# Kernel optimization log

Measured on AMD Instinct MI355X. Metric: run time of the kernel, lower is better.

Reference implementation:

```python
import jax, jax.numpy as jnp
import numpy as np

N = 50000   # nodes
E = 800000  # edges (avg degree 16)
H = 256     # hidden_dim
OUT = 256   # out_dim


def _leaky(x, slope=0.01):
    return jnp.where(x >= 0, x, slope * x)


def _mlp3(x, W1, b1, W2, b2, W3, b3):
    # MLP(hidden, hidden/2, hidden/2, hidden) with LeakyReLU(0.01) between layers
    x = _leaky(x @ W1 + b1)
    x = _leaky(x @ W2 + b2)
    return x @ W3 + b3


def setup_inputs() -> dict:
    key = jax.random.key(0)
    ks = jax.random.split(key, 16)
    Hh = H // 2

    def w(k, i, o):
        return (jax.random.normal(k, (i, o), jnp.float32) / np.float32(np.sqrt(i)))

    return {
        'h': jax.random.normal(ks[0], (N, H), jnp.float32),
        'src': jax.random.randint(ks[1], (E,), 0, N, dtype=jnp.int32),
        'dst': jax.random.randint(ks[2], (E,), 0, N, dtype=jnp.int32),
        'r': jax.random.randint(ks[3], (E,), 0, 2, dtype=jnp.int32),
        'inv': jax.random.randint(ks[4], (N,), 0, 2, dtype=jnp.int32),
        'inv_W1': w(ks[5], H, Hh), 'inv_b1': jnp.zeros((Hh,), jnp.float32),
        'inv_W2': w(ks[6], Hh, Hh), 'inv_b2': jnp.zeros((Hh,), jnp.float32),
        'inv_W3': w(ks[7], Hh, H), 'inv_b3': jnp.zeros((H,), jnp.float32),
        'and_W1': w(ks[8], H, Hh), 'and_b1': jnp.zeros((Hh,), jnp.float32),
        'and_W2': w(ks[9], Hh, Hh), 'and_b2': jnp.zeros((Hh,), jnp.float32),
        'and_W3': w(ks[10], Hh, H), 'and_b3': jnp.zeros((H,), jnp.float32),
        'proj_W1': w(ks[11], H, H), 'proj_b1': jnp.zeros((H,), jnp.float32),
        'proj_W2': w(ks[12], H, OUT), 'proj_b2': jnp.zeros((OUT,), jnp.float32),
    }


def reference(h, src, dst, r, inv,
              inv_W1, inv_b1, inv_W2, inv_b2, inv_W3, inv_b3,
              and_W1, and_b1, and_W2, and_b2, and_W3, and_b3,
              proj_W1, proj_b1, proj_W2, proj_b2):
    # edge_msg: gather src features, apply func_inv on edges with r == 1
    msg = h[src]  # [E, H]
    msg = jnp.where((r == 1)[:, None],
                    _mlp3(msg, inv_W1, inv_b1, inv_W2, inv_b2, inv_W3, inv_b3),
                    msg)
    # fn.mean('m', 'neigh'): mean over incoming edges per destination node
    sums = jax.ops.segment_sum(msg, dst, num_segments=N)          # [N, H]
    cnt = jax.ops.segment_sum(jnp.ones((E,), msg.dtype), dst, num_segments=N)
    neigh = sums / jnp.maximum(cnt, 1.0)[:, None]
    # apply_nodes_func: func_and, then func_inv where inv flag set
    res = _mlp3(neigh, and_W1, and_b1, and_W2, and_b2, and_W3, and_b3)
    res = jnp.where((inv == 1)[:, None],
                    _mlp3(res, inv_W1, inv_b1, inv_W2, inv_b2, inv_W3, inv_b3),
                    res)
    # proj_head: MLP(H, H, OUT) with negative_slope=0 (i.e. ReLU)
    out = jax.nn.relu(res @ proj_W1 + proj_b1) @ proj_W2 + proj_b2
    return out
```

## Files before the change

### kernel.cpp

```cpp
#include <hip/hip_runtime.h>

typedef _Float16 f16_t;
typedef f16_t f16x2 __attribute__((ext_vector_type(2)));
typedef f16_t f16x4 __attribute__((ext_vector_type(4)));
typedef f16_t f16x8 __attribute__((ext_vector_type(8)));
typedef float f32x4 __attribute__((ext_vector_type(4)));
typedef float f32x16 __attribute__((ext_vector_type(16)));

#define MFMA16H(a, b, c) __builtin_amdgcn_mfma_f32_16x16x32_f16(a, b, c, 0, 0, 0)
#define MFMA32H(a, b, c) __builtin_amdgcn_mfma_f32_32x32x16_f16(a, b, c, 0, 0, 0)

__device__ __forceinline__ float leaky01(float v) { return v >= 0.f ? v : 0.01f * v; }

__device__ __forceinline__ void acc_f16x4(float& s0, float& s1, float& s2, float& s3,
                                          f16x4 v)
{
#if __has_builtin(__builtin_amdgcn_fdot2)
    const f16x2 K10 = (f16x2){(f16_t)1.0f, (f16_t)0.0f};
    const f16x2 K01 = (f16x2){(f16_t)0.0f, (f16_t)1.0f};
    f16x2 lo = (f16x2){v.x, v.y};
    f16x2 hi = (f16x2){v.z, v.w};
    s0 = __builtin_amdgcn_fdot2(lo, K10, s0, false);
    s1 = __builtin_amdgcn_fdot2(lo, K01, s1, false);
    s2 = __builtin_amdgcn_fdot2(hi, K10, s2, false);
    s3 = __builtin_amdgcn_fdot2(hi, K01, s3, false);
#else
    s0 += (float)v.x; s1 += (float)v.y; s2 += (float)v.z; s3 += (float)v.w;
#endif
}

#define OFF_IW1 0
#define OFF_IW2 32768
#define OFF_IW3 49152
#define OFF_AW1 81920
#define OFF_AW2 114688
#define OFF_AW3 131072
#define OFF_PW1 163840
#define OFF_PW2 229376
#define OFF_M3  294912
#define WP_TOTAL 311296

template<int KD, int NC>
__device__ __forceinline__ void gemm16(
    const f16_t* __restrict__ a, int sa, const f16_t* __restrict__ B,
    int cb, int qd, int ln, f32x4 (&acc)[2])
{
    acc[0] = (f32x4){0.f, 0.f, 0.f, 0.f};
    acc[1] = acc[0];
#pragma unroll
    for (int k0 = 0; k0 < KD; k0 += 32) {
        int ka = k0 + qd * 8;
        f16x8 b = *(const f16x8*)(B + ((size_t)((k0 >> 5) * 4 + qd) * NC + cb + ln) * 8);
        f16x8 a0 = *(const f16x8*)&a[ln * sa + ka];
        f16x8 a1 = *(const f16x8*)&a[(16 + ln) * sa + ka];
        acc[0] = MFMA16H(a0, b, acc[0]);
        acc[1] = MFMA16H(a1, b, acc[1]);
    }
}

template<int KD, int NC>
__device__ __forceinline__ void gemm32(
    const f16_t* __restrict__ a, int sa, const f16_t* __restrict__ B,
    int cb, int l31, int kh, f32x16 &o)
{
    f32x16 c;
#pragma unroll
    for (int i = 0; i < 16; ++i) c[i] = 0.f;
    const int ar = l31 * sa + kh * 8;
    const int bcol = cb + l31;
#pragma unroll
    for (int kc = 0; kc < KD; kc += 32) {
        f16x8 b0 = *(const f16x8*)(B + ((size_t)((kc >> 3) + kh) * NC + bcol) * 8);
        f16x8 b1 = *(const f16x8*)(B + ((size_t)((kc >> 3) + 2 + kh) * NC + bcol) * 8);
        f16x8 a0 = *(const f16x8*)&a[ar + kc];
        f16x8 a1 = *(const f16x8*)&a[ar + kc + 16];
        c = MFMA32H(a0, b0, c);
        c = MFMA32H(a1, b1, c);
    }
    o = c;
}

template<int ACT>
__device__ __forceinline__ void epi16(
    f32x4 (&acc)[2], const float* __restrict__ bias,
    int cb, int qd, int ln, f16_t* d, int stride)
{
    int col = cb + ln;
    float bb = bias[col];
#pragma unroll
    for (int rt = 0; rt < 2; ++rt)
#pragma unroll
        for (int r = 0; r < 4; ++r) {
            float v = acc[rt][r] + bb;
            if (ACT == 1) v = leaky01(v);
            else if (ACT == 2) v = fmaxf(v, 0.f);
            d[(rt * 16 + qd * 4 + r) * stride + col] = (f16_t)v;
        }
}

template<int ACT>
__device__ __forceinline__ void epi32(
    const f32x16 &a0, const float* __restrict__ bias,
    int cb, int l31, int kh, f16_t* d, int stride)
{
    int col = cb + l31;
    float bb = bias[col];
#pragma unroll
    for (int r = 0; r < 16; ++r) {
        float v = a0[r] + bb;
        if (ACT == 1) v = leaky01(v);
        else if (ACT == 2) v = fmaxf(v, 0.f);
        int row = (r & 3) + 8 * (r >> 2) + 4 * kh;
        d[row * stride + col] = (f16_t)v;
    }
}

__global__ __launch_bounds__(512) void prep_kernel(
    const float* s0, const float* s1, const float* s2, const float* s3,
    const float* s4, const float* s5, const float* s6, const float* s7,
    const float* __restrict__ ib3, f16_t* dst, float* __restrict__ c3f,
    const int* __restrict__ dstE, int* __restrict__ cnt, int E)
{
    const int tid = threadIdx.x;
    const int bid = blockIdx.x;

    if (bid < 1024) {
        const float* srcs[8] = {s0, s1, s2, s3, s4, s5, s6, s7};
        const int lgN[8] = {7, 7, 8, 7, 7, 8, 8, 8};
        const int sz[8]  = {32768, 16384, 32768, 32768, 16384, 32768, 65536, 65536};
        const int off[8] = {OFF_IW1, OFF_IW2, OFF_IW3, OFF_AW1, OFF_AW2, OFF_AW3,
                            OFF_PW1, OFF_PW2};
        int m = bid >> 7;
        int idx = (bid & 127) * 512 + tid;
        if (idx >= sz[m]) return;
        int lg = lgN[m];
        int Nc = 1 << lg;
        int k = idx >> lg;
        int n = idx & (Nc - 1);
        int p = ((k >> 3) * Nc + n) * 8 + (k & 7);
        dst[off[m] + p] = (f16_t)srcs[m][idx];
    } else if (bid < 1056) {
        int idx = (bid - 1024) * 512 + tid;
        int k = idx >> 7, j = idx & 127;
        float s = 0.f;
        for (int t = 0; t < 256; ++t) s += s2[k * 256 + t] * s3[t * 128 + j];
        int p = ((k >> 3) * 128 + j) * 8 + (k & 7);
        dst[OFF_M3 + p] = (f16_t)s;
    } else if (bid == 1056) {
        int j = tid;
        if (j < 128) {
            float s = 0.f;
            for (int t = 0; t < 256; ++t) s += ib3[t] * s3[t * 128 + j];
            c3f[j] = s;
        }
    } else {
        int e = (bid - 1057) * 512 + tid;
        if (e < E) atomicAdd(&cnt[dstE[e]], 1);
    }
}

__global__ void scan1(const int* __restrict__ cnt, int* __restrict__ offs,
                      int* __restrict__ bsum, int Nn)
{
    __shared__ int s[256];
    int tid = threadIdx.x;
    int g = blockIdx.x * 256 + tid;
    int v = (g < Nn) ? cnt[g] : 0;
    s[tid] = v;
    __syncthreads();
    for (int off = 1; off < 256; off <<= 1) {
        int u = (tid >= off) ? s[tid - off] : 0;
        __syncthreads();
        s[tid] += u;
        __syncthreads();
    }
    if (g < Nn) offs[g] = s[tid] - v;
    if (tid == 255) bsum[blockIdx.x] = s[255];
}

__global__ void scan3b(int* __restrict__ offs, const int* __restrict__ bsum,
                       int* __restrict__ cursor, int Nn, int NB)
{
    __shared__ int s[256];
    int tid = threadIdx.x;
    int bid = blockIdx.x;
    int v = (tid < NB) ? bsum[tid] : 0;
    s[tid] = v;
    __syncthreads();
    for (int off = 1; off < 256; off <<= 1) {
        int u = (tid >= off) ? s[tid - off] : 0;
        __syncthreads();
        s[tid] += u;
        __syncthreads();
    }
    int base = (bid > 0) ? s[bid - 1] : 0;
    int g = bid * 256 + tid;
    if (g < Nn) {
        int o = offs[g] + base;
        offs[g] = o;
        cursor[g] = o;
    }
}

__global__ void scan2(int* __restrict__ bsum, int NB)
{
    if (threadIdx.x == 0) {
        int run = 0;
        for (int i = 0; i < NB; ++i) { int v = bsum[i]; bsum[i] = run; run += v; }
    }
}

__global__ void scan3(int* __restrict__ offs, const int* __restrict__ bsum,
                      int* __restrict__ cursor, int Nn)
{
    int g = blockIdx.x * 256 + threadIdx.x;
    if (g < Nn) {
        int o = offs[g] + bsum[blockIdx.x];
        offs[g] = o;
        cursor[g] = o;
    }
}

__global__ __launch_bounds__(512, 8) void fillA(
    const float* __restrict__ h, f16_t* __restrict__ zbuf,
    const f16_t* __restrict__ wp, const float* __restrict__ ib1,
    const float* __restrict__ ib2, const float* __restrict__ c3f, int M,
    int tiles, const int* __restrict__ dstE, const int* __restrict__ srcE,
    const int* __restrict__ rE, int* __restrict__ cursor,
    int* __restrict__ ridx, int E)
{
    __shared__ f16_t X[32][264];
    __shared__ f16_t Y[32][136];

    const int tid = threadIdx.x;

    if ((int)blockIdx.x >= tiles) {
        int e = (blockIdx.x - tiles) * 512 + tid;
        if (e < E) {
            int p = atomicAdd(&cursor[dstE[e]], 1);
            ridx[p] = srcE[e] * 2 + rE[e];
        }
        return;
    }

    const int row0 = blockIdx.x * 32;
    const int lane = tid & 63;
    const int wv = tid >> 6;
    const int qd = lane >> 4;
    const int ln = lane & 15;
    const int cb = wv * 16;
    const int l31 = lane & 31;
    const int kh = lane >> 5;

    {
        const float4* src4 = (const float4*)(h + (size_t)row0 * 256);
#pragma unroll
        for (int i = 0; i < 4; ++i) {
            int q = i * 512 + tid;
            int row = q >> 6;
            int kc = (q & 63) * 4;
            float4 v = make_float4(0.f, 0.f, 0.f, 0.f);
            if (row0 + row < M) v = src4[q];
            *(f16x4*)&X[row][kc] = (f16x4){(f16_t)v.x, (f16_t)v.y, (f16_t)v.z, (f16_t)v.w};
        }
    }
    __syncthreads();

    {
        const bool isz = wv < 4;
        const int cb32 = (wv & 3) * 32;
        const f16_t* Bw = wp + (isz ? OFF_AW1 : OFF_IW1);
        f32x16 z;
        gemm32<256, 128>(&X[0][0], 264, Bw, cb32, l31, kh, z);
        __syncthreads();
        int col = cb32 + l31;
        if (isz) {
#pragma unroll
            for (int r = 0; r < 16; ++r) {
                int lrow = (r & 3) + 8 * (r >> 2) + 4 * kh;
                X[lrow][128 + col] = (f16_t)z[r];
            }
        } else {
            float bb = ib1[col];
#pragma unroll
            for (int r = 0; r < 16; ++r) {
                int lrow = (r & 3) + 8 * (r >> 2) + 4 * kh;
                Y[lrow][col] = (f16_t)leaky01(z[r] + bb);
            }
        }
    }
    __syncthreads();

    f32x4 a4[2];

    gemm16<128, 128>(&Y[0][0], 136, wp + OFF_IW2, cb, qd, ln, a4);
    epi16<1>(a4, ib2, cb, qd, ln, &X[0][0], 264);
    __syncthreads();

    gemm16<128, 128>(&X[0][0], 264, wp + OFF_M3, cb, qd, ln, a4);
    {
        int col = cb + ln;
        float bb = c3f[col];
#pragma unroll
        for (int rt = 0; rt < 2; ++rt)
#pragma unroll
            for (int r = 0; r < 4; ++r)
                Y[rt * 16 + qd * 4 + r][col] = (f16_t)(a4[rt][r] + bb);
    }
    __syncthreads();

#pragma unroll
    for (int i = 0; i < 2; ++i) {
        int q = i * 512 + tid;
        int node = q >> 5;
        int seg = q & 31;
        int row = row0 + node;
        if (row < M) {
            f16x8 v = (seg < 16) ? *(const f16x8*)&X[node][128 + seg * 8]
                                 : *(const f16x8*)&Y[node][(seg - 16) * 8];
            *(f16x8*)&zbuf[(size_t)row * 256 + seg * 8] = v;
        }
    }
}

__global__ __launch_bounds__(512, 8) void kernelB(
    const f16_t* __restrict__ zbuf, const int* __restrict__ ridx,
    const int* __restrict__ offs, const int* __restrict__ cnt,
    const float* __restrict__ ab1, const int* __restrict__ invf,
    float* __restrict__ out, const f16_t* __restrict__ wp,
    const float* __restrict__ ab2, const float* __restrict__ ab3,
    const float* __restrict__ ib1, const float* __restrict__ ib2,
    const float* __restrict__ ib3, const float* __restrict__ pb1,
    const float* __restrict__ pb2, int M)
{
    __shared__ f16_t C[32][264];
    __shared__ f16_t A[32][136];
    __shared__ f16_t B2[32][136];
    __shared__ int sflag[32];

    const int tid = threadIdx.x;
    const int row0 = blockIdx.x * 32;
    const int lane = tid & 63;
    const int wv = tid >> 6;
    const int qd = lane >> 4;
    const int ln = lane & 15;
    const int cb2 = wv * 16;
    const int l31 = lane & 31;
    const int kh = lane >> 5;
    const int cb32 = wv * 32;

    const int hw = tid >> 5;
    const int hl = tid & 31;
    const int hbase = lane & 32;
    const f16x4* zp4 = (const f16x4*)zbuf;

#pragma unroll
    for (int pass = 0; pass < 2; ++pass) {
        int nl = pass * 16 + hw;
        int row = row0 + nl;
        float s0 = 0.f, s1 = 0.f, s2 = 0.f, s3 = 0.f;
        int c = 0;
        if (row < M) {
            int beg = offs[row];
            c = cnt[row];
            for (int base = 0; base < c; base += 32) {
                int rem = c - base; if (rem > 32) rem = 32;
                int myr = (hl < rem) ? ridx[beg + base + hl] : 0;
                int j = 0;
                for (; j + 16 <= rem; j += 16) {
                    f16x4 v[16];
#pragma unroll
                    for (int i = 0; i < 16; ++i) {
                        int rr = __shfl(myr, hbase + j + i);
                        v[i] = zp4[(size_t)rr * 32 + hl];
                    }
#pragma unroll
                    for (int i = 0; i < 16; ++i)
                        acc_f16x4(s0, s1, s2, s3, v[i]);
                }
                for (; j + 8 <= rem; j += 8) {
                    f16x4 v[8];
#pragma unroll
                    for (int i = 0; i < 8; ++i) {
                        int rr = __shfl(myr, hbase + j + i);
                        v[i] = zp4[(size_t)rr * 32 + hl];
                    }
#pragma unroll
                    for (int i = 0; i < 8; ++i)
                        acc_f16x4(s0, s1, s2, s3, v[i]);
                }
                for (; j < rem; ++j) {
                    int rr = __shfl(myr, hbase + j);
                    f16x4 vv = zp4[(size_t)rr * 32 + hl];
                    acc_f16x4(s0, s1, s2, s3, vv);
                }
            }
        }
        float invc = 1.0f / fmaxf((float)c, 1.0f);
        float4 bv = *(const float4*)&ab1[hl * 4];
        float m0 = leaky01(s0 * invc + bv.x);
        float m1 = leaky01(s1 * invc + bv.y);
        float m2 = leaky01(s2 * invc + bv.z);
        float m3 = leaky01(s3 * invc + bv.w);
        *(f16x4*)&A[nl][hl * 4] = (f16x4){(f16_t)m0, (f16_t)m1, (f16_t)m2, (f16_t)m3};
    }
    if (tid < 32) {
        int rr = row0 + tid;
        sflag[tid] = (rr < M) ? invf[rr] : 0;
    }
    __syncthreads();

    f32x4 a4[2];
    f32x16 c32;

    gemm16<128, 128>(&A[0][0], 136, wp + OFF_AW2, cb2, qd, ln, a4);
    epi16<1>(a4, ab2, cb2, qd, ln, &B2[0][0], 136);
    __syncthreads();

    gemm32<128, 256>(&B2[0][0], 136, wp + OFF_AW3, cb32, l31, kh, c32);
    epi32<0>(c32, ab3, cb32, l31, kh, &C[0][0], 264);
    __syncthreads();

    gemm16<256, 128>(&C[0][0], 264, wp + OFF_IW1, cb2, qd, ln, a4);
    epi16<1>(a4, ib1, cb2, qd, ln, &A[0][0], 136);
    __syncthreads();

    gemm16<128, 128>(&A[0][0], 136, wp + OFF_IW2, cb2, qd, ln, a4);
    epi16<1>(a4, ib2, cb2, qd, ln, &B2[0][0], 136);
    __syncthreads();

    gemm32<128, 256>(&B2[0][0], 136, wp + OFF_IW3, cb32, l31, kh, c32);
    {
        int col = cb32 + l31;
        float bb = ib3[col];
#pragma unroll
        for (int r = 0; r < 16; ++r) {
            int lrow = (r & 3) + 8 * (r >> 2) + 4 * kh;
            if (sflag[lrow] == 1) C[lrow][col] = (f16_t)(c32[r] + bb);
        }
    }
    __syncthreads();

    gemm32<256, 256>(&C[0][0], 264, wp + OFF_PW1, cb32, l31, kh, c32);
    __syncthreads();
    epi32<2>(c32, pb1, cb32, l31, kh, &C[0][0], 264);
    __syncthreads();

    gemm32<256, 256>(&C[0][0], 264, wp + OFF_PW2, cb32, l31, kh, c32);
    {
        int col = cb32 + l31;
        float bb = pb2[col];
#pragma unroll
        for (int r = 0; r < 16; ++r) {
            int lrow = (r & 3) + 8 * (r >> 2) + 4 * kh;
            int row = row0 + lrow;
            if (row < M) out[(size_t)row * 256 + col] = c32[r] + bb;
        }
    }
}

extern "C" void kernel_launch(void* const* d_in, const int* in_sizes, int n_in,
                              void* d_out, int out_size, void* d_ws, size_t ws_size,
                              hipStream_t stream)
{
    const float* h   = (const float*)d_in[0];
    const int* src   = (const int*)d_in[1];
    const int* dst   = (const int*)d_in[2];
    const int* r     = (const int*)d_in[3];
    const int* inv   = (const int*)d_in[4];
    const float* iW1 = (const float*)d_in[5];
    const float* ib1 = (const float*)d_in[6];
    const float* iW2 = (const float*)d_in[7];
    const float* ib2 = (const float*)d_in[8];
    const float* iW3 = (const float*)d_in[9];
    const float* ib3 = (const float*)d_in[10];
    const float* aW1 = (const float*)d_in[11];
    const float* ab1 = (const float*)d_in[12];
    const float* aW2 = (const float*)d_in[13];
    const float* ab2 = (const float*)d_in[14];
    const float* aW3 = (const float*)d_in[15];
    const float* ab3 = (const float*)d_in[16];
    const float* pW1 = (const float*)d_in[17];
    const float* pb1 = (const float*)d_in[18];
    const float* pW2 = (const float*)d_in[19];
    const float* pb2 = (const float*)d_in[20];

    const int N = in_sizes[0] / 256;
    const int E = in_sizes[1];
    float* out = (float*)d_out;

    f16_t* zbuf = (f16_t*)d_ws;
    int* cnt    = (int*)(zbuf + (size_t)2 * N * 128);
    int* offs   = cnt + N;
    int* cursor = offs + N;
    int* bsum   = cursor + N;
    int* ridx   = bsum + 256;
    f16_t* wp   = (f16_t*)(ridx + E);
    float* c3f  = (float*)(wp + WP_TOTAL);

    (void)hipMemsetAsync(cnt, 0, (size_t)N * sizeof(int), stream);

    const int tiles = (N + 31) / 32;
    const int EB = (E + 511) / 512;
    const int NB = (N + 255) / 256;

    prep_kernel<<<1057 + EB, 512, 0, stream>>>(iW1, iW2, iW3, aW1, aW2, aW3,
                                               pW1, pW2, ib3, wp, c3f,
                                               dst, cnt, E);

    scan1<<<NB, 256, 0, stream>>>(cnt, offs, bsum, N);
    if (NB <= 256) {
        scan3b<<<NB, 256, 0, stream>>>(offs, bsum, cursor, N, NB);
    } else {
        scan2<<<1, 1, 0, stream>>>(bsum, NB);
        scan3<<<NB, 256, 0, stream>>>(offs, bsum, cursor, N);
    }

    fillA<<<tiles + EB, 512, 0, stream>>>(h, zbuf, wp, ib1, ib2, c3f, N,
                                          tiles, dst, src, r, cursor, ridx, E);

    kernelB<<<tiles, 512, 0, stream>>>(zbuf, ridx, offs, cnt, ab1, inv, out, wp,
                                       ab2, ab3, ib1, ib2, ib3, pb1, pb2, N);
}
```

Baseline: 323.0 us.

## Fuse all stages into one persistent cooperative kernel with grid syncs

Replaces the memset, prep, scan and two compute kernel launches with a single cooperative persistent kernel. Stages are separated by grid-wide syncs, and work units are distributed with grid-stride loops. The scan now uses 512-thread blocks. The intent is to remove per-launch overhead and inter-kernel gaps. In exchange, occupancy is capped at resident blocks, grid.sync costs are added, and the shared-memory union may limit occupancy. The old multi-kernel path is kept as a fallback.

```diff
diff --git a/kernel.cpp b/kernel.cpp
--- a/kernel.cpp
+++ b/kernel.cpp
@@ -1,4 +1,5 @@
 #include <hip/hip_runtime.h>
+#include <hip/hip_cooperative_groups.h>
 
 typedef _Float16 f16_t;
 typedef f16_t f16x2 __attribute__((ext_vector_type(2)));
@@ -115,15 +116,229 @@
     }
 }
 
-__global__ __launch_bounds__(512) void prep_kernel(
+__device__ __forceinline__ void kernelA_tile(
+    int tile, const float* __restrict__ h, f16_t* __restrict__ zbuf,
+    const f16_t* __restrict__ wp, const float* __restrict__ ib1,
+    const float* __restrict__ ib2, const float* __restrict__ c3f, int M,
+    f16_t (*X)[264], f16_t (*Y)[136], int tid)
+{
+    const int row0 = tile * 32;
+    const int lane = tid & 63;
+    const int wv = tid >> 6;
+    const int qd = lane >> 4;
+    const int ln = lane & 15;
+    const int cb = wv * 16;
+    const int l31 = lane & 31;
+    const int kh = lane >> 5;
+
+    {
+        const float4* src4 = (const float4*)(h + (size_t)row0 * 256);
+#pragma unroll
+        for (int i = 0; i < 4; ++i) {
+            int q = i * 512 + tid;
+            int row = q >> 6;
+            int kc = (q & 63) * 4;
+            float4 v = make_float4(0.f, 0.f, 0.f, 0.f);
+            if (row0 + row < M) v = src4[q];
+            *(f16x4*)&X[row][kc] = (f16x4){(f16_t)v.x, (f16_t)v.y, (f16_t)v.z, (f16_t)v.w};
+        }
+    }
+    __syncthreads();
+
+    {
+        const bool isz = wv < 4;
+        const int cb32 = (wv & 3) * 32;
+        const f16_t* Bw = wp + (isz ? OFF_AW1 : OFF_IW1);
+        f32x16 z;
+        gemm32<256, 128>(&X[0][0], 264, Bw, cb32, l31, kh, z);
+        __syncthreads();
+        int col = cb32 + l31;
+        if (isz) {
+#pragma unroll
+            for (int r = 0; r < 16; ++r) {
+                int lrow = (r & 3) + 8 * (r >> 2) + 4 * kh;
+                X[lrow][128 + col] = (f16_t)z[r];
+            }
+        } else {
+            float bb = ib1[col];
+#pragma unroll
+            for (int r = 0; r < 16; ++r) {
+                int lrow = (r & 3) + 8 * (r >> 2) + 4 * kh;
+                Y[lrow][col] = (f16_t)leaky01(z[r] + bb);
+            }
+        }
+    }
+    __syncthreads();
+
+    f32x4 a4[2];
+
+    gemm16<128, 128>(&Y[0][0], 136, wp + OFF_IW2, cb, qd, ln, a4);
+    epi16<1>(a4, ib2, cb, qd, ln, &X[0][0], 264);
+    __syncthreads();
+
+    gemm16<128, 128>(&X[0][0], 264, wp + OFF_M3, cb, qd, ln, a4);
+    {
+        int col = cb + ln;
+        float bb = c3f[col];
+#pragma unroll
+        for (int rt = 0; rt < 2; ++rt)
+#pragma unroll
+            for (int r = 0; r < 4; ++r)
+                Y[rt * 16 + qd * 4 + r][col] = (f16_t)(a4[rt][r] + bb);
+    }
+    __syncthreads();
+
+#pragma unroll
+    for (int i = 0; i < 2; ++i) {
+        int q = i * 512 + tid;
+        int node = q >> 5;
+        int seg = q & 31;
+        int row = row0 + node;
+        if (row < M) {
+            f16x8 v = (seg < 16) ? *(const f16x8*)&X[node][128 + seg * 8]
+                                 : *(const f16x8*)&Y[node][(seg - 16) * 8];
+            *(f16x8*)&zbuf[(size_t)row * 256 + seg * 8] = v;
+        }
+    }
+}
+
+__device__ __forceinline__ void kernelB_tile(
+    int tile, const f16_t* __restrict__ zbuf, const int* __restrict__ ridx,
+    const int* __restrict__ offs, const int* __restrict__ cnt,
+    const float* __restrict__ ab1, const int* __restrict__ invf,
+    float* __restrict__ out, const f16_t* __restrict__ wp,
+    const float* __restrict__ ab2, const float* __restrict__ ab3,
+    const float* __restrict__ ib1, const float* __restrict__ ib2,
+    const float* __restrict__ ib3, const float* __restrict__ pb1,
+    const float* __restrict__ pb2, int M,
+    f16_t (*C)[264], f16_t (*A)[136], f16_t (*B2)[136], int* sflag, int tid)
+{
+    const int row0 = tile * 32;
+    const int lane = tid & 63;
+    const int wv = tid >> 6;
+    const int qd = lane >> 4;
+    const int ln = lane & 15;
+    const int cb2 = wv * 16;
+    const int l31 = lane & 31;
+    const int kh = lane >> 5;
+    const int cb32 = wv * 32;
+
+    const int hw = tid >> 5;
+    const int hl = tid & 31;
+    const int hbase = lane & 32;
+    const f16x4* zp4 = (const f16x4*)zbuf;
+
+#pragma unroll
+    for (int pass = 0; pass < 2; ++pass) {
+        int nl = pass * 16 + hw;
+        int row = row0 + nl;
+        float s0 = 0.f, s1 = 0.f, s2 = 0.f, s3 = 0.f;
+        int c = 0;
+        if (row < M) {
+            int beg = offs[row];
+            c = cnt[row];
+            for (int base = 0; base < c; base += 32) {
+                int rem = c - base; if (rem > 32) rem = 32;
+                int myr = (hl < rem) ? ridx[beg + base + hl] : 0;
+                int j = 0;
+                for (; j + 16 <= rem; j += 16) {
+                    f16x4 v[16];
+#pragma unroll
+                    for (int i = 0; i < 16; ++i) {
+                        int rr = __shfl(myr, hbase + j + i);
+                        v[i] = zp4[(size_t)rr * 32 + hl];
+                    }
+#pragma unroll
+                    for (int i = 0; i < 16; ++i)
+                        acc_f16x4(s0, s1, s2, s3, v[i]);
+                }
+                for (; j + 8 <= rem; j += 8) {
+                    f16x4 v[8];
+#pragma unroll
+                    for (int i = 0; i < 8; ++i) {
+                        int rr = __shfl(myr, hbase + j + i);
+                        v[i] = zp4[(size_t)rr * 32 + hl];
+                    }
+#pragma unroll
+                    for (int i = 0; i < 8; ++i)
+                        acc_f16x4(s0, s1, s2, s3, v[i]);
+                }
+                for (; j < rem; ++j) {
+                    int rr = __shfl(myr, hbase + j);
+                    f16x4 vv = zp4[(size_t)rr * 32 + hl];
+                    acc_f16x4(s0, s1, s2, s3, vv);
+                }
+            }
+        }
+        float invc = 1.0f / fmaxf((float)c, 1.0f);
+        float4 bv = *(const float4*)&ab1[hl * 4];
+        float m0 = leaky01(s0 * invc + bv.x);
+        float m1 = leaky01(s1 * invc + bv.y);
+        float m2 = leaky01(s2 * invc + bv.z);
+        float m3 = leaky01(s3 * invc + bv.w);
+        *(f16x4*)&A[nl][hl * 4] = (f16x4){(f16_t)m0, (f16_t)m1, (f16_t)m2, (f16_t)m3};
+    }
+    if (tid < 32) {
+        int rr = row0 + tid;
+        sflag[tid] = (rr < M) ? invf[rr] : 0;
+    }
+    __syncthreads();
+
+    f32x4 a4[2];
+    f32x16 c32;
+
+    gemm16<128, 128>(&A[0][0], 136, wp + OFF_AW2, cb2, qd, ln, a4);
+    epi16<1>(a4, ab2, cb2, qd, ln, &B2[0][0], 136);
+    __syncthreads();
+
+    gemm32<128, 256>(&B2[0][0], 136, wp + OFF_AW3, cb32, l31, kh, c32);
+    epi32<0>(c32, ab3, cb32, l31, kh, &C[0][0], 264);
+    __syncthreads();
+
+    gemm16<256, 128>(&C[0][0], 264, wp + OFF_IW1, cb2, qd, ln, a4);
+    epi16<1>(a4, ib1, cb2, qd, ln, &A[0][0], 136);
+    __syncthreads();
+
+    gemm16<128, 128>(&A[0][0], 136, wp + OFF_IW2, cb2, qd, ln, a4);
+    epi16<1>(a4, ib2, cb2, qd, ln, &B2[0][0], 136);
+    __syncthreads();
+
+    gemm32<128, 256>(&B2[0][0], 136, wp + OFF_IW3, cb32, l31, kh, c32);
+    {
+        int col = cb32 + l31;
+        float bb = ib3[col];
+#pragma unroll
+        for (int r = 0; r < 16; ++r) {
+            int lrow = (r & 3) + 8 * (r >> 2) + 4 * kh;
+            if (sflag[lrow] == 1) C[lrow][col] = (f16_t)(c32[r] + bb);
+        }
+    }
+    __syncthreads();
+
+    gemm32<256, 256>(&C[0][0], 264, wp + OFF_PW1, cb32, l31, kh, c32);
+    __syncthreads();
+    epi32<2>(c32, pb1, cb32, l31, kh, &C[0][0], 264);
+    __syncthreads();
+
+    gemm32<256, 256>(&C[0][0], 264, wp + OFF_PW2, cb32, l31, kh, c32);
+    {
+        int col = cb32 + l31;
+        float bb = pb2[col];
+#pragma unroll
+        for (int r = 0; r < 16; ++r) {
+            int lrow = (r & 3) + 8 * (r >> 2) + 4 * kh;
+            int row = row0 + lrow;
+            if (row < M) out[(size_t)row * 256 + col] = c32[r] + bb;
+        }
+    }
+}
+
+__device__ __forceinline__ void prep_unit(
+    int bid, int tid,
     const float* s0, const float* s1, const float* s2, const float* s3,
     const float* s4, const float* s5, const float* s6, const float* s7,
-    const float* __restrict__ ib3, f16_t* dst, float* __restrict__ c3f,
-    const int* __restrict__ dstE, int* __restrict__ cnt, int E)
-{
-    const int tid = threadIdx.x;
-    const int bid = blockIdx.x;
-
+    const float* __restrict__ ib3, f16_t* dst, float* __restrict__ c3f)
+{
     if (bid < 1024) {
         const float* srcs[8] = {s0, s1, s2, s3, s4, s5, s6, s7};
         const int lgN[8] = {7, 7, 8, 7, 7, 8, 8, 8};
@@ -153,6 +368,131 @@
             for (int t = 0; t < 256; ++t) s += ib3[t] * s3[t * 128 + j];
             c3f[j] = s;
         }
+    }
+}
+
+struct MegaArgs {
+    const float *h;
+    const float *iW1, *ib1, *iW2, *ib2, *iW3, *ib3;
+    const float *aW1, *ab1, *aW2, *ab2, *aW3, *ab3;
+    const float *pW1, *pb1, *pW2, *pb2;
+    const int *src, *dst, *r, *invf;
+    f16_t *zbuf;
+    f16_t *wp;
+    float *c3f;
+    float *out;
+    int *cnt, *offs, *cursor, *bsum, *ridx;
+    int N, E, tiles, EB, NBc;
+};
+
+__global__ __launch_bounds__(512, 8) void mega(MegaArgs a)
+{
+    namespace cg = cooperative_groups;
+    cg::grid_group grid = cg::this_grid();
+    __shared__ union {
+        struct { f16_t X[32][264]; f16_t Y[32][136]; } pa;
+        struct { f16_t C[32][264]; f16_t A[32][136]; f16_t B2[32][136]; int sflag[32]; } pb;
+        int s[512];
+    } sh;
+    const int tid = threadIdx.x;
+    const int nb = gridDim.x;
+
+    for (int i = blockIdx.x * 512 + tid; i < a.N; i += nb * 512) a.cnt[i] = 0;
+    __threadfence();
+    grid.sync();
+
+    {
+        const int T1 = 1057 + a.EB;
+        for (int u = blockIdx.x; u < T1; u += nb) {
+            if (u < 1057) {
+                prep_unit(u, tid, a.iW1, a.iW2, a.iW3, a.aW1, a.aW2, a.aW3,
+                          a.pW1, a.pW2, a.ib3, a.wp, a.c3f);
+            } else {
+                int e = (u - 1057) * 512 + tid;
+                if (e < a.E) atomicAdd(&a.cnt[a.dst[e]], 1);
+            }
+        }
+    }
+    __threadfence();
+    grid.sync();
+
+    for (int u = blockIdx.x; u < a.NBc; u += nb) {
+        __syncthreads();
+        int g = u * 512 + tid;
+        int v = (g < a.N) ? a.cnt[g] : 0;
+        sh.s[tid] = v;
+        __syncthreads();
+        for (int off = 1; off < 512; off <<= 1) {
+            int t = (tid >= off) ? sh.s[tid - off] : 0;
+            __syncthreads();
+            sh.s[tid] += t;
+            __syncthreads();
+        }
+        if (g < a.N) a.offs[g] = sh.s[tid] - v;
+        if (tid == 511) a.bsum[u] = sh.s[511];
+    }
+    __threadfence();
+    grid.sync();
+
+    for (int u = blockIdx.x; u < a.NBc; u += nb) {
+        __syncthreads();
+        int v = (tid < a.NBc) ? a.bsum[tid] : 0;
+        sh.s[tid] = v;
+        __syncthreads();
+        for (int off = 1; off < 512; off <<= 1) {
+            int t = (tid >= off) ? sh.s[tid - off] : 0;
+            __syncthreads();
+            sh.s[tid] += t;
+            __syncthreads();
+        }
+        int base = (u > 0) ? sh.s[u - 1] : 0;
+        int g = u * 512 + tid;
+        if (g < a.N) {
+            int o = a.offs[g] + base;
+            a.offs[g] = o;
+            a.cursor[g] = o;
+        }
+    }
+    __threadfence();
+    grid.sync();
+
+    {
+        const int T4 = a.EB + a.tiles;
+        for (int u = blockIdx.x; u < T4; u += nb) {
+            if (u < a.EB) {
+                int e = u * 512 + tid;
+                if (e < a.E) {
+                    int p = atomicAdd(&a.cursor[a.dst[e]], 1);
+                    a.ridx[p] = a.src[e] * 2 + a.r[e];
+                }
+            } else {
+                __syncthreads();
+                kernelA_tile(u - a.EB, a.h, a.zbuf, a.wp, a.ib1, a.ib2, a.c3f,
+                             a.N, sh.pa.X, sh.pa.Y, tid);
+            }
+        }
+    }
+    __threadfence();
+    grid.sync();
+
+    for (int u = blockIdx.x; u < a.tiles; u += nb) {
+        __syncthreads();
+        kernelB_tile(u, a.zbuf, a.ridx, a.offs, a.cnt, a.ab1, a.invf, a.out,
+                     a.wp, a.ab2, a.ab3, a.ib1, a.ib2, a.ib3, a.pb1, a.pb2,
+                     a.N, sh.pb.C, sh.pb.A, sh.pb.B2, sh.pb.sflag, tid);
+    }
+}
+
+__global__ __launch_bounds__(512) void prep_kernel(
+    const float* s0, const float* s1, const float* s2, const float* s3,
+    const float* s4, const float* s5, const float* s6, const float* s7,
+    const float* __restrict__ ib3, f16_t* dst, float* __restrict__ c3f,
+    const int* __restrict__ dstE, int* __restrict__ cnt, int E)
+{
+    const int tid = threadIdx.x;
+    const int bid = blockIdx.x;
+    if (bid < 1057) {
+        prep_unit(bid, tid, s0, s1, s2, s3, s4, s5, s6, s7, ib3, dst, c3f);
     } else {
         int e = (bid - 1057) * 512 + tid;
         if (e < E) atomicAdd(&cnt[dstE[e]], 1);
@@ -231,9 +571,7 @@
 {
     __shared__ f16_t X[32][264];
     __shared__ f16_t Y[32][136];
-
     const int tid = threadIdx.x;
-
     if ((int)blockIdx.x >= tiles) {
         int e = (blockIdx.x - tiles) * 512 + tid;
         if (e < E) {
@@ -242,85 +580,7 @@
         }
         return;
     }
-
-    const int row0 = blockIdx.x * 32;
-    const int lane = tid & 63;
-    const int wv = tid >> 6;
-    const int qd = lane >> 4;
-    const int ln = lane & 15;
-    const int cb = wv * 16;
-    const int l31 = lane & 31;
-    const int kh = lane >> 5;
-
-    {
-        const float4* src4 = (const float4*)(h + (size_t)row0 * 256);
-#pragma unroll
-        for (int i = 0; i < 4; ++i) {
-            int q = i * 512 + tid;
-            int row = q >> 6;
-            int kc = (q & 63) * 4;
-            float4 v = make_float4(0.f, 0.f, 0.f, 0.f);
-            if (row0 + row < M) v = src4[q];
-            *(f16x4*)&X[row][kc] = (f16x4){(f16_t)v.x, (f16_t)v.y, (f16_t)v.z, (f16_t)v.w};
-        }
-    }
-    __syncthreads();
-
-    {
-        const bool isz = wv < 4;
-        const int cb32 = (wv & 3) * 32;
-        const f16_t* Bw = wp + (isz ? OFF_AW1 : OFF_IW1);
-        f32x16 z;
-        gemm32<256, 128>(&X[0][0], 264, Bw, cb32, l31, kh, z);
-        __syncthreads();
-        int col = cb32 + l31;
-        if (isz) {
-#pragma unroll
-            for (int r = 0; r < 16; ++r) {
-                int lrow = (r & 3) + 8 * (r >> 2) + 4 * kh;
-                X[lrow][128 + col] = (f16_t)z[r];
-            }
-        } else {
-            float bb = ib1[col];
-#pragma unroll
-            for (int r = 0; r < 16; ++r) {
-                int lrow = (r & 3) + 8 * (r >> 2) + 4 * kh;
-                Y[lrow][col] = (f16_t)leaky01(z[r] + bb);
-            }
-        }
-    }
-    __syncthreads();
-
-    f32x4 a4[2];
-
-    gemm16<128, 128>(&Y[0][0], 136, wp + OFF_IW2, cb, qd, ln, a4);
-    epi16<1>(a4, ib2, cb, qd, ln, &X[0][0], 264);
-    __syncthreads();
-
-    gemm16<128, 128>(&X[0][0], 264, wp + OFF_M3, cb, qd, ln, a4);
-    {
-        int col = cb + ln;
-        float bb = c3f[col];
-#pragma unroll
-        for (int rt = 0; rt < 2; ++rt)
-#pragma unroll
-            for (int r = 0; r < 4; ++r)
-                Y[rt * 16 + qd * 4 + r][col] = (f16_t)(a4[rt][r] + bb);
-    }
-    __syncthreads();
-
-#pragma unroll
-    for (int i = 0; i < 2; ++i) {
-        int q = i * 512 + tid;
-        int node = q >> 5;
-        int seg = q & 31;
-        int row = row0 + node;
-        if (row < M) {
-            f16x8 v = (seg < 16) ? *(const f16x8*)&X[node][128 + seg * 8]
-                                 : *(const f16x8*)&Y[node][(seg - 16) * 8];
-            *(f16x8*)&zbuf[(size_t)row * 256 + seg * 8] = v;
-        }
-    }
+    kernelA_tile(blockIdx.x, h, zbuf, wp, ib1, ib2, c3f, M, X, Y, tid);
 }
 
 __global__ __launch_bounds__(512, 8) void kernelB(
@@ -337,126 +597,9 @@
     __shared__ f16_t A[32][136];
     __shared__ f16_t B2[32][136];
     __shared__ int sflag[32];
-
-    const int tid = threadIdx.x;
-    const int row0 = blockIdx.x * 32;
-    const int lane = tid & 63;
-    const int wv = tid >> 6;
-    const int qd = lane >> 4;
-    const int ln = lane & 15;
-    const int cb2 = wv * 16;
-    const int l31 = lane & 31;
-    const int kh = lane >> 5;
-    const int cb32 = wv * 32;
-
-    const int hw = tid >> 5;
-    const int hl = tid & 31;
-    const int hbase = lane & 32;
-    const f16x4* zp4 = (const f16x4*)zbuf;
-
-#pragma unroll
-    for (int pass = 0; pass < 2; ++pass) {
-        int nl = pass * 16 + hw;
-        int row = row0 + nl;
-        float s0 = 0.f, s1 = 0.f, s2 = 0.f, s3 = 0.f;
-        int c = 0;
-        if (row < M) {
-            int beg = offs[row];
-            c = cnt[row];
-            for (int base = 0; base < c; base += 32) {
-                int rem = c - base; if (rem > 32) rem = 32;
-                int myr = (hl < rem) ? ridx[beg + base + hl] : 0;
-                int j = 0;
-                for (; j + 16 <= rem; j += 16) {
-                    f16x4 v[16];
-#pragma unroll
-                    for (int i = 0; i < 16; ++i) {
-                        int rr = __shfl(myr, hbase + j + i);
-                        v[i] = zp4[(size_t)rr * 32 + hl];
-                    }
-#pragma unroll
-                    for (int i = 0; i < 16; ++i)
-                        acc_f16x4(s0, s1, s2, s3, v[i]);
-                }
-                for (; j + 8 <= rem; j += 8) {
-                    f16x4 v[8];
-#pragma unroll
-                    for (int i = 0; i < 8; ++i) {
-                        int rr = __shfl(myr, hbase + j + i);
-                        v[i] = zp4[(size_t)rr * 32 + hl];
-                    }
-#pragma unroll
-                    for (int i = 0; i < 8; ++i)
-                        acc_f16x4(s0, s1, s2, s3, v[i]);
-                }
-                for (; j < rem; ++j) {
-                    int rr = __shfl(myr, hbase + j);
-                    f16x4 vv = zp4[(size_t)rr * 32 + hl];
-                    acc_f16x4(s0, s1, s2, s3, vv);
-                }
-            }
-        }
-        float invc = 1.0f / fmaxf((float)c, 1.0f);
-        float4 bv = *(const float4*)&ab1[hl * 4];
-        float m0 = leaky01(s0 * invc + bv.x);
-        float m1 = leaky01(s1 * invc + bv.y);
-        float m2 = leaky01(s2 * invc + bv.z);
-        float m3 = leaky01(s3 * invc + bv.w);
-        *(f16x4*)&A[nl][hl * 4] = (f16x4){(f16_t)m0, (f16_t)m1, (f16_t)m2, (f16_t)m3};
-    }
-    if (tid < 32) {
-        int rr = row0 + tid;
-        sflag[tid] = (rr < M) ? invf[rr] : 0;
-    }
-    __syncthreads();
-
-    f32x4 a4[2];
-    f32x16 c32;
-
-    gemm16<128, 128>(&A[0][0], 136, wp + OFF_AW2, cb2, qd, ln, a4);
-    epi16<1>(a4, ab2, cb2, qd, ln, &B2[0][0], 136);
-    __syncthreads();
-
-    gemm32<128, 256>(&B2[0][0], 136, wp + OFF_AW3, cb32, l31, kh, c32);
-    epi32<0>(c32, ab3, cb32, l31, kh, &C[0][0], 264);
-    __syncthreads();
-
-    gemm16<256, 128>(&C[0][0], 264, wp + OFF_IW1, cb2, qd, ln, a4);
-    epi16<1>(a4, ib1, cb2, qd, ln, &A[0][0], 136);
-    __syncthreads();
-
-    gemm16<128, 128>(&A[0][0], 136, wp + OFF_IW2, cb2, qd, ln, a4);
-    epi16<1>(a4, ib2, cb2, qd, ln, &B2[0][0], 136);
-    __syncthreads();
-
-    gemm32<128, 256>(&B2[0][0], 136, wp + OFF_IW3, cb32, l31, kh, c32);
-    {
-        int col = cb32 + l31;
-        float bb = ib3[col];
-#pragma unroll
-        for (int r = 0; r < 16; ++r) {
-            int lrow = (r & 3) + 8 * (r >> 2) + 4 * kh;
-            if (sflag[lrow] == 1) C[lrow][col] = (f16_t)(c32[r] + bb);
-        }
-    }
-    __syncthreads();
-
-    gemm32<256, 256>(&C[0][0], 264, wp + OFF_PW1, cb32, l31, kh, c32);
-    __syncthreads();
-    epi32<2>(c32, pb1, cb32, l31, kh, &C[0][0], 264);
-    __syncthreads();
-
-    gemm32<256, 256>(&C[0][0], 264, wp + OFF_PW2, cb32, l31, kh, c32);
-    {
-        int col = cb32 + l31;
-        float bb = pb2[col];
-#pragma unroll
-        for (int r = 0; r < 16; ++r) {
-            int lrow = (r & 3) + 8 * (r >> 2) + 4 * kh;
-            int row = row0 + lrow;
-            if (row < M) out[(size_t)row * 256 + col] = c32[r] + bb;
-        }
-    }
+    kernelB_tile(blockIdx.x, zbuf, ridx, offs, cnt, ab1, invf, out, wp,
+                 ab2, ab3, ib1, ib2, ib3, pb1, pb2, M, C, A, B2, sflag,
+                 threadIdx.x);
 }
 
 extern "C" void kernel_launch(void* const* d_in, const int* in_sizes, int n_in,
@@ -498,27 +641,55 @@
     f16_t* wp   = (f16_t*)(ridx + E);
     float* c3f  = (float*)(wp + WP_TOTAL);
 
-    (void)hipMemsetAsync(cnt, 0, (size_t)N * sizeof(int), stream);
-
     const int tiles = (N + 31) / 32;
     const int EB = (E + 511) / 512;
     const int NB = (N + 255) / 256;
-
-    prep_kernel<<<1057 + EB, 512, 0, stream>>>(iW1, iW2, iW3, aW1, aW2, aW3,
-                                               pW1, pW2, ib3, wp, c3f,
-                                               dst, cnt, E);
-
-    scan1<<<NB, 256, 0, stream>>>(cnt, offs, bsum, N);
-    if (NB <= 256) {
-        scan3b<<<NB, 256, 0, stream>>>(offs, bsum, cursor, N, NB);
-    } else {
-        scan2<<<1, 1, 0, stream>>>(bsum, NB);
-        scan3<<<NB, 256, 0, stream>>>(offs, bsum, cursor, N);
-    }
-
-    fillA<<<tiles + EB, 512, 0, stream>>>(h, zbuf, wp, ib1, ib2, c3f, N,
-                                          tiles, dst, src, r, cursor, ridx, E);
-
-    kernelB<<<tiles, 512, 0, stream>>>(zbuf, ridx, offs, cnt, ab1, inv, out, wp,
-                                       ab2, ab3, ib1, ib2, ib3, pb1, pb2, N);
-}
+    const int NBc = (N + 511) / 512;
+
+    static int coopBlocks = -2;
+    if (coopBlocks == -2) {
+        int maxB = 0;
+        hipError_t qe = hipOccupancyMaxActiveBlocksPerMultiprocessor(&maxB, mega, 512, 0);
+        coopBlocks = (qe == hipSuccess && maxB > 0) ? maxB * 256 : -1;
+    }
+
+    bool done = false;
+    if (coopBlocks > 0 && NBc <= 512 && NBc <= 256 ) {
+        MegaArgs a;
+        a.h = h; a.iW1 = iW1; a.ib1 = ib1; a.iW2 = iW2; a.ib2 = ib2;
+        a.iW3 = iW3; a.ib3 = ib3; a.aW1 = aW1; a.ab1 = ab1; a.aW2 = aW2;
+        a.ab2 = ab2; a.aW3 = aW3; a.ab3 = ab3; a.pW1 = pW1; a.pb1 = pb1;
+        a.pW2 = pW2; a.pb2 = pb2;
+        a.src = src; a.dst = dst; a.r = r; a.invf = inv;
+        a.zbuf = zbuf; a.wp = wp; a.c3f = c3f; a.out = out;
+        a.cnt = cnt; a.offs = offs; a.cursor = cursor; a.bsum = bsum; a.ridx = ridx;
+        a.N = N; a.E = E; a.tiles = tiles; a.EB = EB; a.NBc = NBc;
+        void* params[] = {&a};
+        hipError_t err = hipLaunchCooperativeKernel(mega, dim3(coopBlocks),
+                                                    dim3(512), params, 0, stream);
+        if (err == hipSuccess) {
+            done = true;
+        } else {
+            coopBlocks = -1;
+            (void)hipGetLastError();
+        }
+    }
+
+    if (!done) {
+        (void)hipMemsetAsync(cnt, 0, (size_t)N * sizeof(int), stream);
+        prep_kernel<<<1057 + EB, 512, 0, stream>>>(iW1, iW2, iW3, aW1, aW2, aW3,
+                                                   pW1, pW2, ib3, wp, c3f,
+                                                   dst, cnt, E);
+        scan1<<<NB, 256, 0, stream>>>(cnt, offs, bsum, N);
+        if (NB <= 256) {
+            scan3b<<<NB, 256, 0, stream>>>(offs, bsum, cursor, N, NB);
+        } else {
+            scan2<<<1, 1, 0, stream>>>(bsum, NB);
+            scan3<<<NB, 256, 0, stream>>>(offs, bsum, cursor, N);
+        }
+        fillA<<<tiles + EB, 512, 0, stream>>>(h, zbuf, wp, ib1, ib2, c3f, N,
+                                              tiles, dst, src, r, cursor, ridx, E);
+        kernelB<<<tiles, 512, 0, stream>>>(zbuf, ridx, offs, cnt, ab1, inv, out, wp,
+                                           ab2, ab3, ib1, ib2, ib3, pb1, pb2, N);
+    }
+}
```

After: 1.262 ms. +290.6%, slower.
